# Kernel tuning notes

Measured on AMD Instinct MI355X. Metric: run time of the kernel, lower is better.

Reference implementation:

```python
import jax, jax.numpy as jnp
import numpy as np

N_NODES = 50000
N_EDGES = 600000
IN_DIM = 128
OUT_DIM = 128
N_REL = 32
N_BASES = 4
BN_EPS = 1e-5


def setup_inputs() -> dict:
    key = jax.random.key(0)
    ks = jax.random.split(key, 8)
    entity_emb = jax.random.normal(ks[0], (N_NODES, IN_DIM), dtype=jnp.float32)
    bases = jax.random.normal(ks[1], (N_BASES, IN_DIM, OUT_DIM), dtype=jnp.float32) * 0.05
    coefficients = jax.random.normal(ks[2], (N_REL, N_BASES), dtype=jnp.float32) * 0.5
    W_loop = jax.random.normal(ks[3], (IN_DIM, OUT_DIM), dtype=jnp.float32) * 0.05
    b_loop = jnp.zeros((OUT_DIM,), dtype=jnp.float32)
    gamma = jnp.ones((OUT_DIM,), dtype=jnp.float32)
    beta = jnp.zeros((OUT_DIM,), dtype=jnp.float32)
    edge_index = jax.random.randint(ks[4], (2, N_EDGES), 0, N_NODES, dtype=jnp.int32)
    edge_type = jax.random.randint(ks[5], (N_EDGES,), 0, N_REL, dtype=jnp.int32)
    return {"entity_emb": entity_emb, "bases": bases, "coefficients": coefficients,
            "W_loop": W_loop, "b_loop": b_loop, "gamma": gamma, "beta": beta,
            "edge_index": edge_index, "edge_type": edge_type}


def reference(entity_emb, bases, coefficients, W_loop, b_loop, gamma, beta, edge_index, edge_type):
    N = entity_emb.shape[0]
    # self-loop linear
    out = entity_emb @ W_loop + b_loop  # [N, out_dim]
    # basis decomposition: per-relation weight W[r] = sum_b coeff[r,b] * bases[b]
    W = jnp.einsum('rb,bio->rio', coefficients, bases)  # [R, in, out]
    src, dst = edge_index[0], edge_index[1]
    # per-edge message: entity_emb[src_e] @ W[edge_type_e]  (vectorizes the per-relation loop)
    msg = jnp.einsum('ei,eio->eo', entity_emb[src], W[edge_type])  # [E, out]
    out = out + jax.ops.segment_sum(msg, dst, num_segments=N)
    # degree normalization (in-degree over all edges, clamped at 1)
    deg = jax.ops.segment_sum(jnp.ones_like(dst, dtype=out.dtype), dst, num_segments=N)
    out = out / jnp.maximum(deg, 1.0)[:, None]
    # BatchNorm1d (training mode: biased batch stats over node dim)
    mean = jnp.mean(out, axis=0)
    var = jnp.mean((out - mean) ** 2, axis=0)
    out = (out - mean) / jnp.sqrt(var + BN_EPS) * gamma + beta
    return jax.nn.relu(out)
```

## Files before the change

### kernel.cpp

```cpp
#include <hip/hip_runtime.h>
#include <cstdint>

#define NN 50000
#define NE 600000

typedef unsigned short ushort_t;
typedef __bf16 bf16_t;
typedef __attribute__((ext_vector_type(8))) bf16_t bf16x8;
typedef __attribute__((ext_vector_type(8))) ushort_t ushort8;
typedef __attribute__((ext_vector_type(4))) float f32x4;

#define WT_OFF   0ul
#define XG_OFF   40960ul
#define XBF_OFF  16040960ul
#define CNT_OFF  19240960ul
#define CUR_OFF  19290960ul
#define BSUM_OFF 19340960ul
#define BSCN_OFF 19341088ul
#define CS_OFF   19341216ul
#define CSQ_OFF  19341344ul

__device__ __forceinline__ float2 bf2_to_f2(uint32_t u) {
    float2 r;
    r.x = __uint_as_float(u << 16);
    r.y = __uint_as_float(u & 0xffff0000u);
    return r;
}

__device__ __forceinline__ ushort_t f2bf(float f) {
    uint32_t u = __float_as_uint(f);
    u = (u + 0x7fffu + ((u >> 16) & 1u)) >> 16;
    return (ushort_t)u;
}

__device__ __forceinline__ uint32_t f2bf2(float x, float y) {
    return (uint32_t)f2bf(x) | ((uint32_t)f2bf(y) << 16);
}

__device__ __forceinline__ void async_copy16(const void* g, void* l) {
    __builtin_amdgcn_global_load_lds(
        (const __attribute__((address_space(1))) void*)g,
        (__attribute__((address_space(3))) void*)l, 16, 0, 0);
}

__global__ __launch_bounds__(256) void k_prep(
    const float* __restrict__ Wl, const float* __restrict__ bases,
    ushort_t* __restrict__ WT)
{
    const int i = blockIdx.x * 256 + threadIdx.x;
    if (i >= 128 * 640) return;
    const int n = i / 640;
    const int kk = i - n * 640;
    float v;
    if (kk < 128) v = Wl[kk * 128 + n];
    else {
        const int j = kk - 128;
        v = bases[(size_t)(j >> 7) * 16384 + (j & 127) * 128 + n];
    }
    WT[i] = f2bf(v);
}

__global__ __launch_bounds__(256) void k_cast(
    const float* __restrict__ X, ushort_t* __restrict__ Xbf,
    ushort_t* __restrict__ XG)
{
    __shared__ ushort_t L[16][136];
    const int tid = threadIdx.x;
    const int tile = blockIdx.x;
    {
        const int row = tid >> 4, gc = tid & 15;
        const int node = tile * 16 + row;
        const float4* p = (const float4*)(X + (size_t)node * 128 + gc * 8);
        const float4 a = p[0], b = p[1];
        ushort_t t8[8] = { f2bf(a.x), f2bf(a.y), f2bf(a.z), f2bf(a.w),
                           f2bf(b.x), f2bf(b.y), f2bf(b.z), f2bf(b.w) };
        const uint4 v = *(const uint4*)t8;
        *(uint4*)&L[row][gc * 8] = v;
        *(uint4*)(Xbf + (size_t)node * 128 + gc * 8) = v;
    }
    __syncthreads();
    {
        const int g = tid >> 4, r2 = tid & 15;
        const uint4 u = *(const uint4*)&L[r2][g * 8];
        *(uint4*)(XG + (size_t)tile * 10240 + g * 128 + r2 * 8) = u;
    }
}

__global__ __launch_bounds__(256) void k_hist(
    const int* __restrict__ eidx, int* __restrict__ cnt)
{
    const int* __restrict__ dst = eidx + NE;
    for (int e = blockIdx.x * 256 + threadIdx.x; e < NE; e += gridDim.x * 256)
        atomicAdd(cnt + dst[e], 1);
}

__global__ __launch_bounds__(256) void k_scan1(
    const int* __restrict__ cnt, int* __restrict__ curs, int* __restrict__ bsum)
{
    __shared__ int sh[256];
    const int tid = threadIdx.x;
    const int i0 = blockIdx.x * 512 + tid * 2;
    const int v0 = (i0 < NN) ? cnt[i0] : 0;
    const int v1 = (i0 + 1 < NN) ? cnt[i0 + 1] : 0;
    int s = v0 + v1;
    sh[tid] = s;
    __syncthreads();
#pragma unroll
    for (int off = 1; off < 256; off <<= 1) {
        int t = (tid >= off) ? sh[tid - off] : 0;
        __syncthreads();
        sh[tid] += t;
        __syncthreads();
    }
    const int excl = sh[tid] - s;
    if (i0 < NN) curs[i0] = excl;
    if (i0 + 1 < NN) curs[i0 + 1] = excl + v0;
    if (tid == 255) bsum[blockIdx.x] = sh[255];
}

__global__ __launch_bounds__(128) void k_scan2(
    const int* __restrict__ bsum, int* __restrict__ bscan, int nblk)
{
    __shared__ int sh[128];
    const int tid = threadIdx.x;
    int v = (tid < nblk) ? bsum[tid] : 0;
    sh[tid] = v;
    __syncthreads();
#pragma unroll
    for (int off = 1; off < 128; off <<= 1) {
        int t = (tid >= off) ? sh[tid - off] : 0;
        __syncthreads();
        sh[tid] += t;
        __syncthreads();
    }
    if (tid < nblk) bscan[tid] = sh[tid] - v;
}

__global__ __launch_bounds__(256) void k_scan3(
    int* __restrict__ curs, const int* __restrict__ bscan)
{
    const int add = bscan[blockIdx.x];
    const int i0 = blockIdx.x * 512 + threadIdx.x * 2;
    if (i0 < NN) curs[i0] += add;
    if (i0 + 1 < NN) curs[i0 + 1] += add;
}

__global__ __launch_bounds__(256) void k_scatter(
    const int* __restrict__ eidx, const int* __restrict__ etype,
    int* __restrict__ curs, uint32_t* __restrict__ epack)
{
    const int* __restrict__ src = eidx;
    const int* __restrict__ dst = eidx + NE;
    for (int e = blockIdx.x * 256 + threadIdx.x; e < NE; e += gridDim.x * 256) {
        const int d = dst[e];
        const int pos = atomicAdd(curs + d, 1);
        epack[pos] = (uint32_t)src[e] | ((uint32_t)etype[e] << 16);
    }
}

__device__ __forceinline__ void edge_accum8(
    uint32_t ep, const ushort_t* __restrict__ Xbf,
    const float* __restrict__ coeff, int k, float* m)
{
    const int s = ep & 0xffff;
    const int t = ep >> 16;
    const float4 cw = *(const float4*)(coeff + t * 4);
    const uint4 xv = *(const uint4*)(Xbf + (size_t)s * 128 + k * 8);
    float x[8];
    float2 p;
    p = bf2_to_f2(xv.x); x[0] = p.x; x[1] = p.y;
    p = bf2_to_f2(xv.y); x[2] = p.x; x[3] = p.y;
    p = bf2_to_f2(xv.z); x[4] = p.x; x[5] = p.y;
    p = bf2_to_f2(xv.w); x[6] = p.x; x[7] = p.y;
#pragma unroll
    for (int c = 0; c < 8; ++c) {
        m[0 * 8 + c] += cw.x * x[c];
        m[1 * 8 + c] += cw.y * x[c];
        m[2 * 8 + c] += cw.z * x[c];
        m[3 * 8 + c] += cw.w * x[c];
    }
}

__global__ __launch_bounds__(256) void k_gather(
    const ushort_t* __restrict__ Xbf, const uint32_t* __restrict__ epack,
    const int* __restrict__ cnt, const int* __restrict__ curs,
    const float* __restrict__ coeff, ushort_t* __restrict__ XG)
{
    const int lane = threadIdx.x & 63;
    const int w = threadIdx.x >> 6;
    const int sub = lane >> 4;
    const int k = lane & 15;
    const int tile = blockIdx.x;
    const int d = tile * 16 + w * 4 + sub;

    const int n = cnt[d];
    const int end = curs[d];
    int j = end - n;

    float m[32];
#pragma unroll
    for (int i = 0; i < 32; ++i) m[i] = 0.f;

    for (; j + 3 < end; j += 4) {
        const uint32_t e0 = epack[j];
        const uint32_t e1 = epack[j + 1];
        const uint32_t e2 = epack[j + 2];
        const uint32_t e3 = epack[j + 3];
        edge_accum8(e0, Xbf, coeff, k, m);
        edge_accum8(e1, Xbf, coeff, k, m);
        edge_accum8(e2, Xbf, coeff, k, m);
        edge_accum8(e3, Xbf, coeff, k, m);
    }
    for (; j < end; ++j) edge_accum8(epack[j], Xbf, coeff, k, m);

    uint32_t* gb = (uint32_t*)(XG + (size_t)tile * 10240);
#pragma unroll
    for (int b = 0; b < 4; ++b) {
        uint4 v;
        v.x = f2bf2(m[b * 8 + 0], m[b * 8 + 1]);
        v.y = f2bf2(m[b * 8 + 2], m[b * 8 + 3]);
        v.z = f2bf2(m[b * 8 + 4], m[b * 8 + 5]);
        v.w = f2bf2(m[b * 8 + 6], m[b * 8 + 7]);
        *(uint4*)(gb + (16 + b * 16 + k) * 64 + (w * 4 + sub) * 4) = v;
    }
}

__global__ __launch_bounds__(256) void k_gemm_f(
    const ushort_t* __restrict__ XG, const ushort_t* __restrict__ WT,
    const float* __restrict__ bl, const int* __restrict__ cnt,
    float* __restrict__ out, float* __restrict__ colsum,
    float* __restrict__ colsq)
{
    __shared__ ushort_t As[2][10240];
    const int tid = threadIdx.x;
    const int lane = tid & 63;
    const int w = tid >> 6;
    const int row0 = blockIdx.x * 32;
    const int tile0 = blockIdx.x * 2;

#pragma unroll
    for (int k = 0; k < 10; ++k) {
        const int s = w * 10 + k;
        const int tl = s >= 20 ? 1 : 0;
        const int off = s - tl * 20;
        const ushort_t* src = XG + (size_t)(tile0 + tl) * 10240 + off * 512 + lane * 8;
        async_copy16(src, &As[tl][off * 512]);
    }
    __syncthreads();

    const int m = lane & 15;
    const int quad = lane >> 4;
    const ushort_t* bp0 = WT + (size_t)(w * 32 + m) * 640 + quad * 8;
    const ushort_t* bp1 = bp0 + 16 * 640;

    f32x4 cc[2][2];
#pragma unroll
    for (int rt = 0; rt < 2; ++rt)
#pragma unroll
        for (int ct = 0; ct < 2; ++ct)
#pragma unroll
            for (int i = 0; i < 4; ++i) cc[rt][ct][i] = 0.f;

#pragma unroll
    for (int c = 0; c < 20; ++c) {
        const bf16x8 b0 = __builtin_bit_cast(bf16x8, *(const ushort8*)(bp0 + c * 32));
        const bf16x8 b1 = __builtin_bit_cast(bf16x8, *(const ushort8*)(bp1 + c * 32));
        const int aoff = (c * 4 + quad) * 128 + m * 8;
        const bf16x8 a0 = __builtin_bit_cast(bf16x8, *(const ushort8*)&As[0][aoff]);
        const bf16x8 a1 = __builtin_bit_cast(bf16x8, *(const ushort8*)&As[1][aoff]);
        cc[0][0] = __builtin_amdgcn_mfma_f32_16x16x32_bf16(a0, b0, cc[0][0], 0, 0, 0);
        cc[0][1] = __builtin_amdgcn_mfma_f32_16x16x32_bf16(a0, b1, cc[0][1], 0, 0, 0);
        cc[1][0] = __builtin_amdgcn_mfma_f32_16x16x32_bf16(a1, b0, cc[1][0], 0, 0, 0);
        cc[1][1] = __builtin_amdgcn_mfma_f32_16x16x32_bf16(a1, b1, cc[1][1], 0, 0, 0);
    }

    const float blv0 = bl[w * 32 + m];
    const float blv1 = bl[w * 32 + 16 + m];
    float s0 = 0.f, q0 = 0.f, s1 = 0.f, q1 = 0.f;

#pragma unroll
    for (int rt = 0; rt < 2; ++rt) {
        const int rowb = row0 + rt * 16 + quad * 4;
#pragma unroll
        for (int r = 0; r < 4; ++r) {
            const int row = rowb + r;
            if (row < NN) {
                const int dg = cnt[row];
                const float inv = 1.0f / (float)((dg > 0) ? dg : 1);
                float* po = out + (size_t)row * 128 + w * 32 + m;
                const float v0 = (cc[rt][0][r] + blv0) * inv;
                const float v1 = (cc[rt][1][r] + blv1) * inv;
                po[0]  = v0;
                po[16] = v1;
                s0 += v0; q0 += v0 * v0;
                s1 += v1; q1 += v1 * v1;
            }
        }
    }

    s0 += __shfl_down(s0, 32); q0 += __shfl_down(q0, 32);
    s0 += __shfl_down(s0, 16); q0 += __shfl_down(q0, 16);
    s1 += __shfl_down(s1, 32); q1 += __shfl_down(q1, 32);
    s1 += __shfl_down(s1, 16); q1 += __shfl_down(q1, 16);
    if (lane < 16) {
        atomicAdd(colsum + w * 32 + lane, s0);
        atomicAdd(colsq  + w * 32 + lane, q0);
        atomicAdd(colsum + w * 32 + 16 + lane, s1);
        atomicAdd(colsq  + w * 32 + 16 + lane, q1);
    }
}

__global__ __launch_bounds__(256) void k_bn_relu(
    float* __restrict__ out, const float* __restrict__ colsum,
    const float* __restrict__ colsq, const float* __restrict__ gamma,
    const float* __restrict__ beta)
{
    __shared__ float sc[128], sh[128];
    const int tid = threadIdx.x;
    if (tid < 128) {
        const float mean = colsum[tid] * (1.0f / NN);
        const float var = colsq[tid] * (1.0f / NN) - mean * mean;
        const float g = gamma[tid] * rsqrtf(var + 1e-5f);
        sc[tid] = g;
        sh[tid] = beta[tid] - mean * g;
    }
    __syncthreads();
    const int total = NN * 32;
    for (int i = blockIdx.x * 256 + tid; i < total; i += gridDim.x * 256) {
        const int c = (i & 31) << 2;
        float4 v = *(float4*)(out + (size_t)i * 4);
        v.x = fmaxf(fmaf(v.x, sc[c + 0], sh[c + 0]), 0.f);
        v.y = fmaxf(fmaf(v.y, sc[c + 1], sh[c + 1]), 0.f);
        v.z = fmaxf(fmaf(v.z, sc[c + 2], sh[c + 2]), 0.f);
        v.w = fmaxf(fmaf(v.w, sc[c + 3], sh[c + 3]), 0.f);
        *(float4*)(out + (size_t)i * 4) = v;
    }
}

extern "C" void kernel_launch(void* const* d_in, const int* in_sizes, int n_in,
                              void* d_out, int out_size, void* d_ws, size_t ws_size,
                              hipStream_t stream)
{
    const float* X      = (const float*)d_in[0];
    const float* bases  = (const float*)d_in[1];
    const float* coeff  = (const float*)d_in[2];
    const float* Wl     = (const float*)d_in[3];
    const float* bl     = (const float*)d_in[4];
    const float* gamma  = (const float*)d_in[5];
    const float* beta   = (const float*)d_in[6];
    const int*   eidx   = (const int*)d_in[7];
    const int*   etype  = (const int*)d_in[8];
    float* out = (float*)d_out;

    float* ws = (float*)d_ws;
    ushort_t* WT     = (ushort_t*)(ws + WT_OFF);
    ushort_t* XG     = (ushort_t*)(ws + XG_OFF);
    ushort_t* Xbf    = (ushort_t*)(ws + XBF_OFF);
    int*      cnt    = (int*)(ws + CNT_OFF);
    int*      curs   = (int*)(ws + CUR_OFF);
    int*      bsum   = (int*)(ws + BSUM_OFF);
    int*      bscan  = (int*)(ws + BSCN_OFF);
    float*    colsum = ws + CS_OFF;
    float*    colsq  = ws + CSQ_OFF;
    uint32_t* epack  = (uint32_t*)d_out;

    hipMemsetAsync(cnt, 0, (CSQ_OFF + 128 - CNT_OFF) * sizeof(float), stream);

    const int nblk_scan = (NN + 511) / 512;

    k_prep<<<(128 * 640 + 255) / 256, 256, 0, stream>>>(Wl, bases, WT);
    k_cast<<<3125, 256, 0, stream>>>(X, Xbf, XG);
    k_hist<<<512, 256, 0, stream>>>(eidx, cnt);
    k_scan1<<<nblk_scan, 256, 0, stream>>>(cnt, curs, bsum);
    k_scan2<<<1, 128, 0, stream>>>(bsum, bscan, nblk_scan);
    k_scan3<<<nblk_scan, 256, 0, stream>>>(curs, bscan);
    k_scatter<<<512, 256, 0, stream>>>(eidx, etype, curs, epack);
    k_gather<<<3125, 256, 0, stream>>>(Xbf, epack, cnt, curs, coeff, XG);
    k_gemm_f<<<1563, 256, 0, stream>>>(XG, WT, bl, cnt, out, colsum, colsq);
    k_bn_relu<<<1024, 256, 0, stream>>>(out, colsum, colsq, gamma, beta);
}
```

Baseline: 281.1 us.

## Tile GEMM 64 rows per block with double-buffered LDS staging of A and B

```diff
diff --git a/kernel.cpp b/kernel.cpp
--- a/kernel.cpp
+++ b/kernel.cpp
@@ -45,19 +45,24 @@
 
 __global__ __launch_bounds__(256) void k_prep(
     const float* __restrict__ Wl, const float* __restrict__ bases,
-    ushort_t* __restrict__ WT)
+    ushort_t* __restrict__ WTf)
 {
     const int i = blockIdx.x * 256 + threadIdx.x;
-    if (i >= 128 * 640) return;
-    const int n = i / 640;
-    const int kk = i - n * 640;
+    if (i >= 81920) return;
+    const int it = i >> 13;
+    const int r1 = i & 8191;
+    const int q = r1 >> 10;
+    const int r2 = r1 & 1023;
+    const int n = r2 >> 3;
+    const int j = r2 & 7;
+    const int k = it * 64 + q * 8 + j;
     float v;
-    if (kk < 128) v = Wl[kk * 128 + n];
+    if (k < 128) v = Wl[k * 128 + n];
     else {
-        const int j = kk - 128;
-        v = bases[(size_t)(j >> 7) * 16384 + (j & 127) * 128 + n];
-    }
-    WT[i] = f2bf(v);
+        const int jj = k - 128;
+        v = bases[(size_t)(jj >> 7) * 16384 + (jj & 127) * 128 + n];
+    }
+    WTf[i] = f2bf(v);
 }
 
 __global__ __launch_bounds__(256) void k_cast(
@@ -225,88 +230,118 @@
     }
 }
 
+__device__ __forceinline__ void stage_iter(
+    const ushort_t* __restrict__ XG, const ushort_t* __restrict__ WTf,
+    ushort_t* __restrict__ Lbuf, int tile0, int it, int w, int lane)
+{
+#pragma unroll
+    for (int c6 = 0; c6 < 6; ++c6) {
+        const int c = w * 6 + c6;
+        if (c < 8) {
+            const int rt = c >> 1, hf = c & 1;
+            const ushort_t* src = XG + (size_t)(tile0 + rt) * 10240
+                                 + it * 1024 + hf * 512 + lane * 8;
+            async_copy16(src, Lbuf + rt * 1024 + hf * 512);
+        } else {
+            const int cb = c - 8, q = cb >> 1, hf = cb & 1;
+            const ushort_t* src = WTf + it * 8192 + q * 1024 + hf * 512 + lane * 8;
+            async_copy16(src, Lbuf + 4096 + q * 1024 + hf * 512);
+        }
+    }
+}
+
 __global__ __launch_bounds__(256) void k_gemm_f(
-    const ushort_t* __restrict__ XG, const ushort_t* __restrict__ WT,
+    const ushort_t* __restrict__ XG, const ushort_t* __restrict__ WTf,
     const float* __restrict__ bl, const int* __restrict__ cnt,
     float* __restrict__ out, float* __restrict__ colsum,
     float* __restrict__ colsq)
 {
-    __shared__ ushort_t As[2][10240];
+    __shared__ ushort_t L[2][12288];
     const int tid = threadIdx.x;
     const int lane = tid & 63;
     const int w = tid >> 6;
-    const int row0 = blockIdx.x * 32;
-    const int tile0 = blockIdx.x * 2;
-
-#pragma unroll
-    for (int k = 0; k < 10; ++k) {
-        const int s = w * 10 + k;
-        const int tl = s >= 20 ? 1 : 0;
-        const int off = s - tl * 20;
-        const ushort_t* src = XG + (size_t)(tile0 + tl) * 10240 + off * 512 + lane * 8;
-        async_copy16(src, &As[tl][off * 512]);
-    }
-    __syncthreads();
-
+    const int row0 = blockIdx.x * 64;
+    const int tile0 = blockIdx.x * 4;
     const int m = lane & 15;
     const int quad = lane >> 4;
-    const ushort_t* bp0 = WT + (size_t)(w * 32 + m) * 640 + quad * 8;
-    const ushort_t* bp1 = bp0 + 16 * 640;
-
-    f32x4 cc[2][2];
-#pragma unroll
-    for (int rt = 0; rt < 2; ++rt)
-#pragma unroll
-        for (int ct = 0; ct < 2; ++ct)
-#pragma unroll
-            for (int i = 0; i < 4; ++i) cc[rt][ct][i] = 0.f;
-
-#pragma unroll
-    for (int c = 0; c < 20; ++c) {
-        const bf16x8 b0 = __builtin_bit_cast(bf16x8, *(const ushort8*)(bp0 + c * 32));
-        const bf16x8 b1 = __builtin_bit_cast(bf16x8, *(const ushort8*)(bp1 + c * 32));
-        const int aoff = (c * 4 + quad) * 128 + m * 8;
-        const bf16x8 a0 = __builtin_bit_cast(bf16x8, *(const ushort8*)&As[0][aoff]);
-        const bf16x8 a1 = __builtin_bit_cast(bf16x8, *(const ushort8*)&As[1][aoff]);
-        cc[0][0] = __builtin_amdgcn_mfma_f32_16x16x32_bf16(a0, b0, cc[0][0], 0, 0, 0);
-        cc[0][1] = __builtin_amdgcn_mfma_f32_16x16x32_bf16(a0, b1, cc[0][1], 0, 0, 0);
-        cc[1][0] = __builtin_amdgcn_mfma_f32_16x16x32_bf16(a1, b0, cc[1][0], 0, 0, 0);
-        cc[1][1] = __builtin_amdgcn_mfma_f32_16x16x32_bf16(a1, b1, cc[1][1], 0, 0, 0);
-    }
-
-    const float blv0 = bl[w * 32 + m];
-    const float blv1 = bl[w * 32 + 16 + m];
-    float s0 = 0.f, q0 = 0.f, s1 = 0.f, q1 = 0.f;
-
-#pragma unroll
-    for (int rt = 0; rt < 2; ++rt) {
-        const int rowb = row0 + rt * 16 + quad * 4;
+    const int rh = w & 1;
+    const int chh = w >> 1;
+
+    f32x4 acc[2][4];
+#pragma unroll
+    for (int t = 0; t < 2; ++t)
+#pragma unroll
+        for (int ct = 0; ct < 4; ++ct)
+#pragma unroll
+            for (int i = 0; i < 4; ++i) acc[t][ct][i] = 0.f;
+
+    stage_iter(XG, WTf, L[0], tile0, 0, w, lane);
+    __syncthreads();
+
+    for (int it = 0; it < 10; ++it) {
+        const int pb = it & 1;
+        if (it < 9) stage_iter(XG, WTf, L[pb ^ 1], tile0, it + 1, w, lane);
+
+#pragma unroll
+        for (int kc = 0; kc < 2; ++kc) {
+            const int qoff = kc * 4 + quad;
+            bf16x8 a[2], b[4];
+#pragma unroll
+            for (int t = 0; t < 2; ++t)
+                a[t] = __builtin_bit_cast(bf16x8, *(const ushort8*)
+                    &L[pb][(rh * 2 + t) * 1024 + qoff * 128 + m * 8]);
+#pragma unroll
+            for (int ct = 0; ct < 4; ++ct)
+                b[ct] = __builtin_bit_cast(bf16x8, *(const ushort8*)
+                    &L[pb][4096 + qoff * 1024 + (chh * 64 + ct * 16 + m) * 8]);
+#pragma unroll
+            for (int t = 0; t < 2; ++t)
+#pragma unroll
+                for (int ct = 0; ct < 4; ++ct)
+                    acc[t][ct] = __builtin_amdgcn_mfma_f32_16x16x32_bf16(
+                        a[t], b[ct], acc[t][ct], 0, 0, 0);
+        }
+        __syncthreads();
+    }
+
+    float blv[4], ss[4], qq[4];
+#pragma unroll
+    for (int ct = 0; ct < 4; ++ct) {
+        blv[ct] = bl[chh * 64 + ct * 16 + m];
+        ss[ct] = 0.f; qq[ct] = 0.f;
+    }
+
+#pragma unroll
+    for (int t = 0; t < 2; ++t) {
+        const int rowb = row0 + rh * 32 + t * 16 + quad * 4;
 #pragma unroll
         for (int r = 0; r < 4; ++r) {
             const int row = rowb + r;
             if (row < NN) {
                 const int dg = cnt[row];
                 const float inv = 1.0f / (float)((dg > 0) ? dg : 1);
-                float* po = out + (size_t)row * 128 + w * 32 + m;
-                const float v0 = (cc[rt][0][r] + blv0) * inv;
-                const float v1 = (cc[rt][1][r] + blv1) * inv;
-                po[0]  = v0;
-                po[16] = v1;
-                s0 += v0; q0 += v0 * v0;
-                s1 += v1; q1 += v1 * v1;
+                float* po = out + (size_t)row * 128 + chh * 64 + m;
+#pragma unroll
+                for (int ct = 0; ct < 4; ++ct) {
+                    const float v = (acc[t][ct][r] + blv[ct]) * inv;
+                    po[ct * 16] = v;
+                    ss[ct] += v; qq[ct] += v * v;
+                }
             }
         }
     }
 
-    s0 += __shfl_down(s0, 32); q0 += __shfl_down(q0, 32);
-    s0 += __shfl_down(s0, 16); q0 += __shfl_down(q0, 16);
-    s1 += __shfl_down(s1, 32); q1 += __shfl_down(q1, 32);
-    s1 += __shfl_down(s1, 16); q1 += __shfl_down(q1, 16);
+#pragma unroll
+    for (int ct = 0; ct < 4; ++ct) {
+        ss[ct] += __shfl_down(ss[ct], 32); qq[ct] += __shfl_down(qq[ct], 32);
+        ss[ct] += __shfl_down(ss[ct], 16); qq[ct] += __shfl_down(qq[ct], 16);
+    }
     if (lane < 16) {
-        atomicAdd(colsum + w * 32 + lane, s0);
-        atomicAdd(colsq  + w * 32 + lane, q0);
-        atomicAdd(colsum + w * 32 + 16 + lane, s1);
-        atomicAdd(colsq  + w * 32 + 16 + lane, q1);
+#pragma unroll
+        for (int ct = 0; ct < 4; ++ct) {
+            atomicAdd(colsum + chh * 64 + ct * 16 + lane, ss[ct]);
+            atomicAdd(colsq  + chh * 64 + ct * 16 + lane, qq[ct]);
+        }
     }
 }
 
@@ -353,7 +388,7 @@
     float* out = (float*)d_out;
 
     float* ws = (float*)d_ws;
-    ushort_t* WT     = (ushort_t*)(ws + WT_OFF);
+    ushort_t* WTf    = (ushort_t*)(ws + WT_OFF);
     ushort_t* XG     = (ushort_t*)(ws + XG_OFF);
     ushort_t* Xbf    = (ushort_t*)(ws + XBF_OFF);
     int*      cnt    = (int*)(ws + CNT_OFF);
@@ -368,7 +403,7 @@
 
     const int nblk_scan = (NN + 511) / 512;
 
-    k_prep<<<(128 * 640 + 255) / 256, 256, 0, stream>>>(Wl, bases, WT);
+    k_prep<<<(81920 + 255) / 256, 256, 0, stream>>>(Wl, bases, WTf);
     k_cast<<<3125, 256, 0, stream>>>(X, Xbf, XG);
     k_hist<<<512, 256, 0, stream>>>(eidx, cnt);
     k_scan1<<<nblk_scan, 256, 0, stream>>>(cnt, curs, bsum);
@@ -376,6 +411,7 @@
     k_scan3<<<nblk_scan, 256, 0, stream>>>(curs, bscan);
     k_scatter<<<512, 256, 0, stream>>>(eidx, etype, curs, epack);
     k_gather<<<3125, 256, 0, stream>>>(Xbf, epack, cnt, curs, coeff, XG);
-    k_gemm_f<<<1563, 256, 0, stream>>>(XG, WT, bl, cnt, out, colsum, colsq);
+    k_gemm_f<<<(NN + 63) / 64, 256, 0, stream>>>(
+        XG, WTf, bl, cnt, out, colsum, colsq);
     k_bn_relu<<<1024, 256, 0, stream>>>(out, colsum, colsq, gamma, beta);
 }
```

Result: no change. 281.4 us (+0.1%).
